# Kernel optimization log

Hardware: AMD Instinct MI355X
Metric: run time of the kernel (lower is better)

The kernel has to match this reference:

```python
import jax, jax.numpy as jnp
import numpy as np

V = 1024      # token vocab
C = 8         # n_codebooks
T = 256       # seg_len
BP = 4        # block_pairs (n_latent_blocks)
K = 512       # latent_vocab_size (codebook entries)
E = 128       # emb_dim
D = 128       # latent_dim / d_model
BETA = 0.05
NB = 6 * BP   # decoder sequence length = 24
NH = 4
HD = D // NH
FF = 512
R = 8
IN_FLAT = NB * D
OUT = T * C * V
B = 32


def setup_inputs() -> dict:
    key = jax.random.key(0)
    ks = jax.random.split(key, 20)
    n = lambda i, shape, s=0.02: jax.random.normal(ks[i], shape, jnp.float32) * s
    return {
        "tokens_prev": jax.random.randint(ks[0], (B, T, C), 0, V, jnp.int32),
        "tokens_curr": jax.random.randint(ks[1], (B, T, C), 0, V, jnp.int32),
        "tokens_next": jax.random.randint(ks[2], (B, T, C), 0, V, jnp.int32),
        "emb": n(3, (V, E)),
        "conv1_w": n(4, (4 * D, E * C, 3)),
        "conv1_b": jnp.zeros((4 * D,), jnp.float32),
        "conv2_w": n(5, (2 * D, 4 * D, 1)),
        "conv2_b": jnp.zeros((2 * D,), jnp.float32),
        "cb_instru": jax.random.uniform(ks[6], (K, D), jnp.float32, -1.0 / K, 1.0 / K),
        "cb_vocal": jax.random.uniform(ks[7], (K, D), jnp.float32, -1.0 / K, 1.0 / K),
        "pos": n(8, (1, NB, D), 1.0),
        "attn_in_w": n(9, (3 * D, D)),
        "attn_in_b": jnp.zeros((3 * D,), jnp.float32),
        "attn_out_w": n(10, (D, D)),
        "attn_out_b": jnp.zeros((D,), jnp.float32),
        "ln1_g": jnp.ones((D,), jnp.float32),
        "ln1_b": jnp.zeros((D,), jnp.float32),
        "lin1_w": n(11, (FF, D)),
        "lin1_b": jnp.zeros((FF,), jnp.float32),
        "lin2_w": n(12, (D, FF)),
        "lin2_b": jnp.zeros((D,), jnp.float32),
        "ln2_g": jnp.ones((D,), jnp.float32),
        "ln2_b": jnp.zeros((D,), jnp.float32),
        "lora_a": n(13, (R, IN_FLAT), 0.01),
        "lora_b": n(14, (OUT, R), 0.01),
    }


def _conv1d(x, w, b, pad):
    # x: (B, Cin, L), w: (Cout, Cin, Kw)
    y = jax.lax.conv_general_dilated(x, w, window_strides=(1,), padding=[(pad, pad)],
                                     dimension_numbers=("NCH", "OIH", "NCH"))
    return y + b[None, :, None]


def _encode(tokens, emb, w1, b1, w2, b2):
    Bb, Tt, Cc = tokens.shape
    x = emb[tokens].reshape(Bb, Tt, -1).transpose(0, 2, 1)       # (B, C*E, T)
    x = jax.nn.relu(_conv1d(x, w1, b1, 1))                        # (B, 4D, T)
    x = jax.nn.relu(_conv1d(x, w2, b2, 0))                        # (B, 2D, T)
    # AdaptiveAvgPool1d(BP) with T % BP == 0 -> mean over contiguous chunks
    x = x.reshape(Bb, 2 * D, BP, Tt // BP).mean(-1).transpose(0, 2, 1)  # (B, BP, 2D)
    return x[..., :D], x[..., D:]


def _vq(z, codebook):
    # z: (B, N, D); eval-mode VQ (no EMA update)
    Bb, N, Dd = z.shape
    flat = z.reshape(-1, Dd)
    dist = (jnp.sum(flat * flat, axis=1, keepdims=True)
            - 2.0 * flat @ codebook.T
            + jnp.sum(codebook * codebook, axis=1))
    codes = jnp.argmin(dist, axis=1)
    z_q = codebook[codes].reshape(Bb, N, Dd)
    commit = jnp.mean((z - jax.lax.stop_gradient(z_q)) ** 2)
    loss = BETA * commit
    z_q_st = z + jax.lax.stop_gradient(z_q - z)
    return z_q_st, codes.reshape(Bb, N), loss


def _layer_norm(x, g, b):
    mu = x.mean(-1, keepdims=True)
    var = ((x - mu) ** 2).mean(-1, keepdims=True)
    return (x - mu) * jax.lax.rsqrt(var + 1e-5) * g + b


def _tf_layer(x, in_w, in_b, out_w, out_b, g1, b1, w1, bb1, w2, bb2, g2, b2):
    # Post-norm TransformerEncoderLayer (relu, eval/no-dropout). x: (B, S, D)
    Bb, S, Dd = x.shape
    qkv = x @ in_w.T + in_b
    q, k, v = jnp.split(qkv, 3, axis=-1)
    q = q.reshape(Bb, S, NH, HD).transpose(0, 2, 1, 3)
    k = k.reshape(Bb, S, NH, HD).transpose(0, 2, 1, 3)
    v = v.reshape(Bb, S, NH, HD).transpose(0, 2, 1, 3)
    attn = jax.nn.softmax(jnp.einsum("bhsd,bhtd->bhst", q, k) / np.sqrt(HD), axis=-1)
    o = jnp.einsum("bhst,bhtd->bhsd", attn, v).transpose(0, 2, 1, 3).reshape(Bb, S, Dd)
    x = _layer_norm(x + o @ out_w.T + out_b, g1, b1)
    ff = jax.nn.relu(x @ w1.T + bb1) @ w2.T + bb2
    return _layer_norm(x + ff, g2, b2)


def reference(tokens_prev, tokens_curr, tokens_next, emb, conv1_w, conv1_b,
              conv2_w, conv2_b, cb_instru, cb_vocal, pos, attn_in_w, attn_in_b,
              attn_out_w, attn_out_b, ln1_g, ln1_b, lin1_w, lin1_b, lin2_w,
              lin2_b, ln2_g, ln2_b, lora_a, lora_b):
    p_i, p_v = _encode(tokens_prev, emb, conv1_w, conv1_b, conv2_w, conv2_b)
    c_i, c_v = _encode(tokens_curr, emb, conv1_w, conv1_b, conv2_w, conv2_b)
    n_i, n_v = _encode(tokens_next, emb, conv1_w, conv1_b, conv2_w, conv2_b)
    p_i_q, _, l1 = _vq(p_i, cb_instru)
    c_i_q, _, l2 = _vq(c_i, cb_instru)
    n_i_q, _, l3 = _vq(n_i, cb_instru)
    p_v_q, _, l4 = _vq(p_v, cb_vocal)
    c_v_q, _, l5 = _vq(c_v, cb_vocal)
    n_v_q, _, l6 = _vq(n_v, cb_vocal)
    vq_loss = l1 + l2 + l3 + l4 + l5 + l6
    z = jnp.concatenate([p_i_q, p_v_q, c_i_q, c_v_q, n_i_q, n_v_q], axis=1)  # (B, 24, D)
    z = z + pos[:, :z.shape[1], :]
    z = _tf_layer(z, attn_in_w, attn_in_b, attn_out_w, attn_out_b,
                  ln1_g, ln1_b, lin1_w, lin1_b, lin2_w, lin2_b, ln2_g, ln2_b)
    Bb = z.shape[0]
    flat = z.reshape(Bb, -1)
    logits = (flat @ lora_a.T) @ lora_b.T          # (B, T*C*V)
    logits = logits.reshape(Bb, T, C, V)
    logp = jax.nn.log_softmax(logits, axis=-1)
    nll = -jnp.take_along_axis(logp, tokens_curr[..., None].astype(jnp.int32), axis=-1)
    recon_loss = nll.mean()
    total_loss = recon_loss + vq_loss
    return total_loss
```

## Files before the change

### kernel.cpp

```cpp
#include <hip/hip_runtime.h>
#include <hip/hip_bf16.h>
#include <cstdint>
#include <cstddef>

typedef __attribute__((ext_vector_type(8))) short short8;
typedef __attribute__((ext_vector_type(4))) float floatx4;


__device__ __forceinline__ ushort f2bf(float f) {
    union { float f; unsigned int u; } x; x.f = f;
    unsigned int r = (x.u + 0x7fffu + ((x.u >> 16) & 1u)) >> 16;
    return (ushort)r;
}
__device__ __forceinline__ float bf2f(ushort u) {
    union { unsigned int u; float f; } x; x.u = ((unsigned int)u) << 16;
    return x.f;
}

__global__ __launch_bounds__(256) void prep_misc(
    const float* __restrict__ emb, const float* __restrict__ w2,
    const float* __restrict__ cbi, const float* __restrict__ cbv,
    ushort* __restrict__ ebf, ushort* __restrict__ w2bf,
    float* __restrict__ cbiT, float* __restrict__ cbvT, float* __restrict__ accum)
{
    int idx = blockIdx.x * 256 + threadIdx.x;
    if (idx < 2) accum[idx] = 0.f;
    if (idx < 131072) {
        ebf[idx] = f2bf(emb[idx]);
    } else if (idx < 262144) {
        int j = idx - 131072;
        w2bf[j] = f2bf(w2[j]);
    } else if (idx < 327680) {
        int j = idx - 262144;
        cbiT[(j & 127) * 512 + (j >> 7)] = cbi[j];
    } else if (idx < 393216) {
        int j = idx - 327680;
        cbvT[(j & 127) * 512 + (j >> 7)] = cbv[j];
    }
}

__global__ __launch_bounds__(256) void prep_w1(
    const float* __restrict__ w1, ushort* __restrict__ w1bf)
{
    int idx = blockIdx.x * 256 + threadIdx.x;
    int e  = idx & 127;
    int co = (idx >> 7) & 511;
    int cc = (idx >> 16) & 7;
    int kw = idx >> 19;
    w1bf[idx] = f2bf(w1[(co * 1024 + cc * 128 + e) * 3 + kw]);
}

__global__ __launch_bounds__(256) void prep_w_tf(
    const float* __restrict__ aiw, const float* __restrict__ aow,
    const float* __restrict__ l1w, const float* __restrict__ l2w,
    ushort* __restrict__ aiwbf, ushort* __restrict__ aowbf,
    ushort* __restrict__ l1wbf, ushort* __restrict__ l2wbf)
{
    int idx = blockIdx.x * 256 + threadIdx.x;
    if (idx < 49152)        aiwbf[idx]          = f2bf(aiw[idx]);
    else if (idx < 65536)   aowbf[idx - 49152]  = f2bf(aow[idx - 49152]);
    else if (idx < 131072)  l1wbf[idx - 65536]  = f2bf(l1w[idx - 65536]);
    else                    l2wbf[idx - 131072] = f2bf(l2w[idx - 131072]);
}

__global__ __launch_bounds__(256) void conv1_mfma(
    const int* __restrict__ tp, const int* __restrict__ tcu, const int* __restrict__ tn,
    const ushort* __restrict__ ebf, const ushort* __restrict__ w1bf,
    const float* __restrict__ b1, ushort* __restrict__ y1)
{
    constexpr int LDA = 136;
    __shared__ ushort As[64 * LDA];
    __shared__ ushort Bs[128 * LDA];
    const int tid = threadIdx.x;
    const int bx = blockIdx.x;
    const int nb = bx & 3, mb = bx >> 2;
    const int set = mb >> 7, bb = (mb >> 2) & 31, t0 = (mb & 3) << 6;
    const int n0 = nb << 7;
    const int* tok = (set == 0) ? tp : ((set == 1) ? tcu : tn);
    const int w = tid >> 6, lane = tid & 63;
    const int rA = lane & 15, q4 = lane >> 4;

    floatx4 acc[4][2];
    for (int mi = 0; mi < 4; ++mi)
        for (int ni = 0; ni < 2; ++ni)
            acc[mi][ni] = (floatx4)(0.0f);

    const int ch = tid & 15;
    for (int kc = 0; kc < 24; ++kc) {
        const int kw = kc >> 3, cc = kc & 7;
        for (int i = 0; i < 4; ++i) {
            const int row = i * 16 + (tid >> 4);
            const int t = t0 + row + kw - 1;
            uint4 val = make_uint4(0u, 0u, 0u, 0u);
            if (t >= 0 && t < 256) {
                const int token = tok[bb * 2048 + t * 8 + cc];
                val = *(const uint4*)(ebf + token * 128 + ch * 8);
            }
            *(uint4*)(As + row * LDA + ch * 8) = val;
        }
        const ushort* wsrc = w1bf + ((size_t)((kw * 8 + cc) * 512 + n0)) * 128;
        for (int i = 0; i < 8; ++i) {
            const int row = i * 16 + (tid >> 4);
            *(uint4*)(Bs + row * LDA + ch * 8) = *(const uint4*)(wsrc + row * 128 + ch * 8);
        }
        __syncthreads();
        for (int ks = 0; ks < 4; ++ks) {
            const int k0 = ks * 32 + q4 * 8;
            short8 a[4], bf[2];
            for (int mi = 0; mi < 4; ++mi)
                a[mi] = *(const short8*)(As + (mi * 16 + rA) * LDA + k0);
            for (int ni = 0; ni < 2; ++ni)
                bf[ni] = *(const short8*)(Bs + ((w * 2 + ni) * 16 + rA) * LDA + k0);
            for (int mi = 0; mi < 4; ++mi)
                for (int ni = 0; ni < 2; ++ni)
                    acc[mi][ni] = __builtin_amdgcn_mfma_f32_16x16x32_bf16(
                        a[mi], bf[ni], acc[mi][ni], 0, 0, 0);
        }
        __syncthreads();
    }
    for (int ni = 0; ni < 2; ++ni) {
        const int co = n0 + (w * 2 + ni) * 16 + rA;
        const float bias = b1[co];
        for (int mi = 0; mi < 4; ++mi) {
            for (int r = 0; r < 4; ++r) {
                const int t = t0 + mi * 16 + q4 * 4 + r;
                float v = acc[mi][ni][r] + bias;
                v = v > 0.f ? v : 0.f;
                y1[((size_t)(set * 32 + bb) * 256 + t) * 512 + co] = f2bf(v);
            }
        }
    }
}

__global__ __launch_bounds__(256) void conv2_mfma(
    const ushort* __restrict__ y1, const ushort* __restrict__ w2bf,
    const float* __restrict__ b2, float* __restrict__ y2)
{
    constexpr int LDA = 136;
    __shared__ ushort As[64 * LDA];
    __shared__ ushort Bs[128 * LDA];
    __shared__ float pool[128];
    const int tid = threadIdx.x;
    const int bx = blockIdx.x;
    const int nb = bx & 1, mb = bx >> 1;
    const int set = mb >> 7, bb = (mb >> 2) & 31, p = mb & 3, t0 = p << 6;
    const int n0 = nb << 7;
    if (tid < 128) pool[tid] = 0.f;
    const int w = tid >> 6, lane = tid & 63;
    const int rA = lane & 15, q4 = lane >> 4;

    floatx4 acc[4][2];
    for (int mi = 0; mi < 4; ++mi)
        for (int ni = 0; ni < 2; ++ni)
            acc[mi][ni] = (floatx4)(0.0f);

    const size_t arowbase = ((size_t)(set * 32 + bb) * 256 + t0) * 512;
    const int ch = tid & 15;
    for (int kc = 0; kc < 4; ++kc) {
        for (int i = 0; i < 4; ++i) {
            const int row = i * 16 + (tid >> 4);
            *(uint4*)(As + row * LDA + ch * 8) =
                *(const uint4*)(y1 + arowbase + (size_t)row * 512 + kc * 128 + ch * 8);
        }
        for (int i = 0; i < 8; ++i) {
            const int row = i * 16 + (tid >> 4);
            *(uint4*)(Bs + row * LDA + ch * 8) =
                *(const uint4*)(w2bf + (size_t)(n0 + row) * 512 + kc * 128 + ch * 8);
        }
        __syncthreads();
        for (int ks = 0; ks < 4; ++ks) {
            const int k0 = ks * 32 + q4 * 8;
            short8 a[4], bf[2];
            for (int mi = 0; mi < 4; ++mi)
                a[mi] = *(const short8*)(As + (mi * 16 + rA) * LDA + k0);
            for (int ni = 0; ni < 2; ++ni)
                bf[ni] = *(const short8*)(Bs + ((w * 2 + ni) * 16 + rA) * LDA + k0);
            for (int mi = 0; mi < 4; ++mi)
                for (int ni = 0; ni < 2; ++ni)
                    acc[mi][ni] = __builtin_amdgcn_mfma_f32_16x16x32_bf16(
                        a[mi], bf[ni], acc[mi][ni], 0, 0, 0);
        }
        __syncthreads();
    }
    for (int ni = 0; ni < 2; ++ni) {
        const int col = (w * 2 + ni) * 16 + rA;
        const float bias = b2[n0 + col];
        float s = 0.f;
        for (int mi = 0; mi < 4; ++mi)
            for (int r = 0; r < 4; ++r) {
                float v = acc[mi][ni][r] + bias;
                s += v > 0.f ? v : 0.f;
            }
        atomicAdd(&pool[col], s);
    }
    __syncthreads();
    if (tid < 128)
        y2[((size_t)(set * 32 + bb) * 4 + p) * 256 + n0 + tid] = pool[tid] * (1.f / 64.f);
}

__global__ __launch_bounds__(256) void vq_kernel(
    const float* __restrict__ y2, const float* __restrict__ cbiT, const float* __restrict__ cbvT,
    const float* __restrict__ cbi, const float* __restrict__ cbv,
    const float* __restrict__ pos, float* __restrict__ ztr, ushort* __restrict__ xbf,
    float* __restrict__ accum)
{
    const int q = blockIdx.x;
    const int tid = threadIdx.x;
    const int set = q >> 7, bb = (q >> 2) & 31, p = q & 3;
    __shared__ float zloc[256];
    __shared__ float bestv[4];
    __shared__ int   besti[4];
    __shared__ int   code_sh[2];
    __shared__ float wsum2[4];
    zloc[tid] = y2[(size_t)q * 256 + tid];
    __syncthreads();
    const int w = tid >> 6, lane = tid & 63;
    const int half = w >> 1, sub = w & 1;
    const float* cbT = half ? cbvT : cbiT;
    const float* zh = zloc + half * 128;
    float best = 1e30f; int bidx = 0x7fffffff;
    for (int rr = 0; rr < 4; ++rr) {
        const int row = sub * 256 + rr * 64 + lane;
        float d2 = 0.f;
        for (int d = 0; d < 128; ++d) {
            float diff = zh[d] - cbT[d * 512 + row];
            d2 += diff * diff;
        }
        if (d2 < best) { best = d2; bidx = row; }
    }
    for (int off = 32; off > 0; off >>= 1) {
        float ov = __shfl_xor(best, off);
        int   oi = __shfl_xor(bidx, off);
        if (ov < best || (ov == best && oi < bidx)) { best = ov; bidx = oi; }
    }
    if (lane == 0) { bestv[w] = best; besti[w] = bidx; }
    __syncthreads();
    if (tid < 2) {
        float v0 = bestv[tid * 2], v1 = bestv[tid * 2 + 1];
        int   i0 = besti[tid * 2], i1 = besti[tid * 2 + 1];
        code_sh[tid] = (v1 < v0 || (v1 == v0 && i1 < i0)) ? i1 : i0;
    }
    __syncthreads();
    const int hh = tid >> 7, d = tid & 127;
    const int code = code_sh[hh];
    const float* cb = hh ? cbv : cbi;
    const float zq = cb[code * 128 + d];
    const float diff = zloc[hh * 128 + d] - zq;
    float sq = diff * diff;
    for (int off = 32; off > 0; off >>= 1) sq += __shfl_xor(sq, off);
    if (lane == 0) wsum2[w] = sq;
    const int s = (set * 2 + hh) * 4 + p;
    const float val = zq + pos[s * 128 + d];
    ztr[((size_t)bb * 24 + s) * 128 + d] = val;
    xbf[((size_t)bb * 24 + s) * 128 + d] = f2bf(val);
    __syncthreads();
    if (tid == 0) atomicAdd(&accum[0], wsum2[0] + wsum2[1] + wsum2[2] + wsum2[3]);
}

template<int KTOT, int NTOT, int RELU, int OUTBF>
__global__ __launch_bounds__(256) void gemm64_kernel(
    const ushort* __restrict__ A, const ushort* __restrict__ Bw,
    const float* __restrict__ bias, void* __restrict__ Co)
{
    constexpr int NBLK = NTOT / 64;
    constexpr int LDA = 136;
    __shared__ ushort As[64 * LDA];
    __shared__ ushort Bs[64 * LDA];
    const int tid = threadIdx.x;
    const int mblk = blockIdx.x / NBLK, nblk = blockIdx.x % NBLK;
    const int m0 = mblk * 64, n0 = nblk * 64;
    const int w = tid >> 6, lane = tid & 63;
    const int rA = lane & 15, q4 = lane >> 4;
    const int ch = tid & 15, rowst = tid >> 4;

    floatx4 acc[4];
    for (int mi = 0; mi < 4; ++mi) acc[mi] = (floatx4)(0.f);

    for (int kc = 0; kc < KTOT / 128; ++kc) {
        for (int i = 0; i < 4; ++i) {
            const int row = i * 16 + rowst;
            *(uint4*)(As + row * LDA + ch * 8) =
                *(const uint4*)(A + (size_t)(m0 + row) * KTOT + kc * 128 + ch * 8);
            *(uint4*)(Bs + row * LDA + ch * 8) =
                *(const uint4*)(Bw + (size_t)(n0 + row) * KTOT + kc * 128 + ch * 8);
        }
        __syncthreads();
        for (int ks = 0; ks < 4; ++ks) {
            const int k0 = ks * 32 + q4 * 8;
            short8 bfr = *(const short8*)(Bs + (w * 16 + rA) * LDA + k0);
            for (int mi = 0; mi < 4; ++mi) {
                short8 a = *(const short8*)(As + (mi * 16 + rA) * LDA + k0);
                acc[mi] = __builtin_amdgcn_mfma_f32_16x16x32_bf16(a, bfr, acc[mi], 0, 0, 0);
            }
        }
        __syncthreads();
    }
    const int col = n0 + w * 16 + rA;
    const float bs = bias[col];
    for (int mi = 0; mi < 4; ++mi) {
        for (int r = 0; r < 4; ++r) {
            const int row = m0 + mi * 16 + q4 * 4 + r;
            float vv = acc[mi][r] + bs;
            if (RELU) vv = vv > 0.f ? vv : 0.f;
            if (OUTBF) ((ushort*)Co)[(size_t)row * NTOT + col] = f2bf(vv);
            else       ((float*)Co)[(size_t)row * NTOT + col]  = vv;
        }
    }
}

template<int KTOT, int WRITE_F32>
__global__ __launch_bounds__(256) void gemm_ln_kernel(
    const ushort* __restrict__ A, const ushort* __restrict__ Bw,
    const float* __restrict__ bias, const float* __restrict__ resid,
    const float* __restrict__ g, const float* __restrict__ beta,
    ushort* __restrict__ outbf, float* __restrict__ outf)
{
    constexpr int LDA = 136;
    __shared__ ushort As[64 * LDA];
    __shared__ ushort Bs[128 * LDA];
    __shared__ float ps[64 * 4], pq[64 * 4], muv[64], invv[64];
    const int tid = threadIdx.x;
    const int m0 = blockIdx.x * 64;
    const int w = tid >> 6, lane = tid & 63;
    const int rA = lane & 15, q4 = lane >> 4;
    const int ch = tid & 15, rowst = tid >> 4;

    floatx4 acc[4][2];
    for (int mi = 0; mi < 4; ++mi)
        for (int ni = 0; ni < 2; ++ni)
            acc[mi][ni] = (floatx4)(0.f);

    for (int kc = 0; kc < KTOT / 128; ++kc) {
        for (int i = 0; i < 4; ++i) {
            const int row = i * 16 + rowst;
            *(uint4*)(As + row * LDA + ch * 8) =
                *(const uint4*)(A + (size_t)(m0 + row) * KTOT + kc * 128 + ch * 8);
        }
        for (int i = 0; i < 8; ++i) {
            const int row = i * 16 + rowst;
            *(uint4*)(Bs + row * LDA + ch * 8) =
                *(const uint4*)(Bw + (size_t)row * KTOT + kc * 128 + ch * 8);
        }
        __syncthreads();
        for (int ks = 0; ks < 4; ++ks) {
            const int k0 = ks * 32 + q4 * 8;
            short8 a[4], bf[2];
            for (int mi = 0; mi < 4; ++mi)
                a[mi] = *(const short8*)(As + (mi * 16 + rA) * LDA + k0);
            for (int ni = 0; ni < 2; ++ni)
                bf[ni] = *(const short8*)(Bs + ((w * 2 + ni) * 16 + rA) * LDA + k0);
            for (int mi = 0; mi < 4; ++mi)
                for (int ni = 0; ni < 2; ++ni)
                    acc[mi][ni] = __builtin_amdgcn_mfma_f32_16x16x32_bf16(
                        a[mi], bf[ni], acc[mi][ni], 0, 0, 0);
        }
        __syncthreads();
    }
    for (int ni = 0; ni < 2; ++ni) {
        const int col = (w * 2 + ni) * 16 + rA;
        const float bs = bias[col];
        for (int mi = 0; mi < 4; ++mi)
            for (int r = 0; r < 4; ++r) {
                const int row = m0 + mi * 16 + q4 * 4 + r;
                acc[mi][ni][r] += bs + resid[(size_t)row * 128 + col];
            }
    }
    for (int mi = 0; mi < 4; ++mi)
        for (int r = 0; r < 4; ++r) {
            float s  = acc[mi][0][r] + acc[mi][1][r];
            float sq = acc[mi][0][r] * acc[mi][0][r] + acc[mi][1][r] * acc[mi][1][r];
            for (int off = 1; off < 16; off <<= 1) {
                s  += __shfl_xor(s, off);
                sq += __shfl_xor(sq, off);
            }
            if (rA == 0) {
                const int rl = mi * 16 + q4 * 4 + r;
                ps[rl * 4 + w] = s;
                pq[rl * 4 + w] = sq;
            }
        }
    __syncthreads();
    if (tid < 64) {
        float s  = ps[tid * 4] + ps[tid * 4 + 1] + ps[tid * 4 + 2] + ps[tid * 4 + 3];
        float sq = pq[tid * 4] + pq[tid * 4 + 1] + pq[tid * 4 + 2] + pq[tid * 4 + 3];
        float mu = s * (1.f / 128.f);
        float var = sq * (1.f / 128.f) - mu * mu;
        muv[tid] = mu;
        invv[tid] = rsqrtf(var + 1e-5f);
    }
    __syncthreads();
    for (int ni = 0; ni < 2; ++ni) {
        const int col = (w * 2 + ni) * 16 + rA;
        const float gg = g[col], bb = beta[col];
        for (int mi = 0; mi < 4; ++mi)
            for (int r = 0; r < 4; ++r) {
                const int rl = mi * 16 + q4 * 4 + r;
                const int row = m0 + rl;
                float v = (acc[mi][ni][r] - muv[rl]) * invv[rl] * gg + bb;
                outbf[(size_t)row * 128 + col] = f2bf(v);
                if (WRITE_F32) outf[(size_t)row * 128 + col] = v;
            }
    }
}

__global__ __launch_bounds__(64) void attn_kernel(
    const float* __restrict__ qkvb, ushort* __restrict__ obuf)
{
    const int bh = blockIdx.x;
    const int b = bh >> 2, h = bh & 3;
    const int tid = threadIdx.x;
    __shared__ float q[24 * 32], k[24 * 32], v[24 * 32], sc[24 * 24];
    for (int i = 0; i < 12; ++i) {
        const int idx = i * 64 + tid;
        const int s = idx >> 5, d = idx & 31;
        const size_t base = ((size_t)(b * 24 + s)) * 384 + h * 32 + d;
        q[idx] = qkvb[base];
        k[idx] = qkvb[base + 128];
        v[idx] = qkvb[base + 256];
    }
    __syncthreads();
    for (int i = 0; i < 9; ++i) {
        const int e = i * 64 + tid;
        const int si = e / 24, j = e - si * 24;
        float a = 0.f;
        for (int d = 0; d < 32; ++d) a += q[si * 32 + d] * k[j * 32 + d];
        sc[si * 24 + j] = a * 0.17677669529663687f;
    }
    __syncthreads();
    if (tid < 24) {
        float* row = sc + tid * 24;
        float m = row[0];
        for (int j = 1; j < 24; ++j) m = row[j] > m ? row[j] : m;
        float ssum = 0.f;
        for (int j = 0; j < 24; ++j) { float e = __expf(row[j] - m); row[j] = e; ssum += e; }
        float inv = 1.f / ssum;
        for (int j = 0; j < 24; ++j) row[j] *= inv;
    }
    __syncthreads();
    for (int i = 0; i < 12; ++i) {
        const int idx = i * 64 + tid;
        const int s = idx >> 5, d = idx & 31;
        float a = 0.f;
        for (int j = 0; j < 24; ++j) a += sc[s * 24 + j] * v[j * 32 + d];
        obuf[((size_t)(b * 24 + s)) * 128 + h * 32 + d] = f2bf(a);
    }
}

__global__ __launch_bounds__(256) void lora_kernel(
    const ushort* __restrict__ zbf, const float* __restrict__ lora_a,
    float* __restrict__ hbuf)
{
    const int b = blockIdx.x;
    const int tid = threadIdx.x;
    const int w = tid >> 6, lane = tid & 63;
    __shared__ float zl[3072];
    for (int idx = tid; idx < 3072; idx += 256) zl[idx] = bf2f(zbf[(size_t)b * 3072 + idx]);
    __syncthreads();
    for (int rr = 0; rr < 2; ++rr) {
        const int r = w + rr * 4;
        float acc = 0.f;
        for (int idx = lane; idx < 3072; idx += 64)
            acc += lora_a[(size_t)r * 3072 + idx] * zl[idx];
        for (int off = 32; off > 0; off >>= 1) acc += __shfl_xor(acc, off);
        if (lane == 0) hbuf[b * 8 + r] = acc;
    }
}

__global__ __launch_bounds__(256) void logits_kernel(
    const float* __restrict__ hbuf, const float* __restrict__ lora_b,
    const int* __restrict__ tokc, float* __restrict__ accum)
{
    const int tid = threadIdx.x;
    const int tcb = blockIdx.x;
    __shared__ float hl[256];
    __shared__ float wsum[4];
    __shared__ float ltok;
    hl[tid] = hbuf[tid];
    float wr[4][8];
    for (int i = 0; i < 4; ++i) {
        const float4* pw = (const float4*)(lora_b + ((size_t)tcb * 1024 + tid + 256 * i) * 8);
        float4 x = pw[0], y = pw[1];
        wr[i][0] = x.x; wr[i][1] = x.y; wr[i][2] = x.z; wr[i][3] = x.w;
        wr[i][4] = y.x; wr[i][5] = y.y; wr[i][6] = y.z; wr[i][7] = y.w;
    }
    __syncthreads();
    float nll = 0.f;
    for (int bb = 0; bb < 32; ++bb) {
        const int tv = tokc[bb * 2048 + tcb];
        const float* h = hl + bb * 8;
        float h0 = h[0], h1 = h[1], h2 = h[2], h3 = h[3];
        float h4 = h[4], h5 = h[5], h6 = h[6], h7 = h[7];
        float sl = 0.f;
        for (int i = 0; i < 4; ++i) {
            float lg = h0 * wr[i][0] + h1 * wr[i][1] + h2 * wr[i][2] + h3 * wr[i][3]
                     + h4 * wr[i][4] + h5 * wr[i][5] + h6 * wr[i][6] + h7 * wr[i][7];
            sl += __expf(lg);
            if (tid + 256 * i == tv) ltok = lg;
        }
        for (int off = 32; off > 0; off >>= 1) sl += __shfl_xor(sl, off);
        if ((tid & 63) == 0) wsum[tid >> 6] = sl;
        __syncthreads();
        if (tid == 0) nll += logf(wsum[0] + wsum[1] + wsum[2] + wsum[3]) - ltok;
        __syncthreads();
    }
    if (tid == 0) atomicAdd(&accum[1], nll);
}

__global__ void finalize_kernel(const float* __restrict__ accum, float* __restrict__ out) {
    out[0] = accum[1] * (1.f / 65536.f) + 0.05f * accum[0] * (1.f / 16384.f);
}

extern "C" void kernel_launch(void* const* d_in, const int* in_sizes, int n_in,
                              void* d_out, int out_size, void* d_ws, size_t ws_size,
                              hipStream_t stream) {
    const int*   tp   = (const int*)d_in[0];
    const int*   tcu  = (const int*)d_in[1];
    const int*   tn   = (const int*)d_in[2];
    const float* emb  = (const float*)d_in[3];
    const float* w1   = (const float*)d_in[4];
    const float* b1   = (const float*)d_in[5];
    const float* w2   = (const float*)d_in[6];
    const float* b2   = (const float*)d_in[7];
    const float* cbi  = (const float*)d_in[8];
    const float* cbv  = (const float*)d_in[9];
    const float* pos  = (const float*)d_in[10];
    const float* aiw  = (const float*)d_in[11];
    const float* aib  = (const float*)d_in[12];
    const float* aow  = (const float*)d_in[13];
    const float* aob  = (const float*)d_in[14];
    const float* g1   = (const float*)d_in[15];
    const float* be1  = (const float*)d_in[16];
    const float* l1w  = (const float*)d_in[17];
    const float* l1b  = (const float*)d_in[18];
    const float* l2w  = (const float*)d_in[19];
    const float* l2b  = (const float*)d_in[20];
    const float* g2   = (const float*)d_in[21];
    const float* be2  = (const float*)d_in[22];
    const float* lra  = (const float*)d_in[23];
    const float* lrb  = (const float*)d_in[24];

    char* wsb = (char*)d_ws;
    ushort* ebf  = (ushort*)(wsb + 0);
    ushort* w1bf = (ushort*)(wsb + 262144);
    ushort* w2bf = (ushort*)(wsb + 3407872);
    float*  cbiT = (float*)(wsb + 3670016);
    float*  cbvT = (float*)(wsb + 3932160);
    ushort* y1   = (ushort*)(wsb + 4194304);
    float*  y2   = (float*)(wsb + 29360128);
    float*  ztr  = (float*)(wsb + 29753344);
    float*  hbuf = (float*)(wsb + 30146560);
    float*  accum= (float*)(wsb + 30147584);
    ushort* aiwbf= (ushort*)(wsb + 30147648);
    ushort* aowbf= (ushort*)(wsb + 30245952);
    ushort* l1wbf= (ushort*)(wsb + 30278720);
    ushort* l2wbf= (ushort*)(wsb + 30409792);
    if (ws_size < 30540864) return;

    float*  qkvb = (float*)(wsb + 4194304);
    ushort* obuf = (ushort*)(wsb + 5373952);
    ushort* x1bf = (ushort*)(wsb + 5570560);
    float*  x1f  = (float*)(wsb + 5767168);
    ushort* hff  = (ushort*)(wsb + 6160384);
    ushort* zbf  = (ushort*)(wsb + 6946816);
    ushort* xbf  = (ushort*)(wsb + 7143424);

    prep_misc<<<1536, 256, 0, stream>>>(emb, w2, cbi, cbv, ebf, w2bf, cbiT, cbvT, accum);
    prep_w1<<<6144, 256, 0, stream>>>(w1, w1bf);
    prep_w_tf<<<768, 256, 0, stream>>>(aiw, aow, l1w, l2w, aiwbf, aowbf, l1wbf, l2wbf);
    conv1_mfma<<<1536, 256, 0, stream>>>(tp, tcu, tn, ebf, w1bf, b1, y1);
    conv2_mfma<<<768, 256, 0, stream>>>(y1, w2bf, b2, y2);
    vq_kernel<<<384, 256, 0, stream>>>(y2, cbiT, cbvT, cbi, cbv, pos, ztr, xbf, accum);
    gemm64_kernel<128, 384, 0, 0><<<72, 256, 0, stream>>>(xbf, aiwbf, aib, qkvb);
    attn_kernel<<<128, 64, 0, stream>>>(qkvb, obuf);
    gemm_ln_kernel<128, 1><<<12, 256, 0, stream>>>(obuf, aowbf, aob, ztr, g1, be1, x1bf, x1f);
    gemm64_kernel<128, 512, 1, 1><<<96, 256, 0, stream>>>(x1bf, l1wbf, l1b, hff);
    gemm_ln_kernel<512, 0><<<12, 256, 0, stream>>>(hff, l2wbf, l2b, x1f, g2, be2, zbf, nullptr);
    lora_kernel<<<32, 256, 0, stream>>>(zbf, lra, hbuf);
    logits_kernel<<<2048, 256, 0, stream>>>(hbuf, lrb, tcu, accum);
    finalize_kernel<<<1, 1, 0, stream>>>(accum, (float*)d_out);
}
```

Measured before the change: 438.6 us.

## Merge prep kernels, enlarge conv tiles with shared embeddings, vectorize VQ, fuse finalize

```diff
diff --git a/kernel.cpp b/kernel.cpp
--- a/kernel.cpp
+++ b/kernel.cpp
@@ -17,113 +17,118 @@
     return x.f;
 }
 
-__global__ __launch_bounds__(256) void prep_misc(
-    const float* __restrict__ emb, const float* __restrict__ w2,
-    const float* __restrict__ cbi, const float* __restrict__ cbv,
-    ushort* __restrict__ ebf, ushort* __restrict__ w2bf,
-    float* __restrict__ cbiT, float* __restrict__ cbvT, float* __restrict__ accum)
+__global__ __launch_bounds__(256) void prep_all(
+    const float* __restrict__ emb, const float* __restrict__ w1,
+    const float* __restrict__ w2, const float* __restrict__ cbi,
+    const float* __restrict__ cbv, const float* __restrict__ aiw,
+    const float* __restrict__ aow, const float* __restrict__ l1w,
+    const float* __restrict__ l2w,
+    ushort* __restrict__ ebf, ushort* __restrict__ w1bf, ushort* __restrict__ w2bf,
+    float* __restrict__ cbiT, float* __restrict__ cbvT,
+    ushort* __restrict__ aiwbf, ushort* __restrict__ aowbf,
+    ushort* __restrict__ l1wbf, ushort* __restrict__ l2wbf,
+    float* __restrict__ accum)
 {
     int idx = blockIdx.x * 256 + threadIdx.x;
-    if (idx < 2) accum[idx] = 0.f;
+    if (idx < 4) accum[idx] = 0.f;
     if (idx < 131072) {
         ebf[idx] = f2bf(emb[idx]);
     } else if (idx < 262144) {
-        int j = idx - 131072;
-        w2bf[j] = f2bf(w2[j]);
+        int j = idx - 131072; w2bf[j] = f2bf(w2[j]);
     } else if (idx < 327680) {
-        int j = idx - 262144;
-        cbiT[(j & 127) * 512 + (j >> 7)] = cbi[j];
+        int j = idx - 262144; cbiT[(j & 127) * 512 + (j >> 7)] = cbi[j];
     } else if (idx < 393216) {
-        int j = idx - 327680;
-        cbvT[(j & 127) * 512 + (j >> 7)] = cbv[j];
-    }
-}
-
-__global__ __launch_bounds__(256) void prep_w1(
-    const float* __restrict__ w1, ushort* __restrict__ w1bf)
-{
-    int idx = blockIdx.x * 256 + threadIdx.x;
-    int e  = idx & 127;
-    int co = (idx >> 7) & 511;
-    int cc = (idx >> 16) & 7;
-    int kw = idx >> 19;
-    w1bf[idx] = f2bf(w1[(co * 1024 + cc * 128 + e) * 3 + kw]);
-}
-
-__global__ __launch_bounds__(256) void prep_w_tf(
-    const float* __restrict__ aiw, const float* __restrict__ aow,
-    const float* __restrict__ l1w, const float* __restrict__ l2w,
-    ushort* __restrict__ aiwbf, ushort* __restrict__ aowbf,
-    ushort* __restrict__ l1wbf, ushort* __restrict__ l2wbf)
-{
-    int idx = blockIdx.x * 256 + threadIdx.x;
-    if (idx < 49152)        aiwbf[idx]          = f2bf(aiw[idx]);
-    else if (idx < 65536)   aowbf[idx - 49152]  = f2bf(aow[idx - 49152]);
-    else if (idx < 131072)  l1wbf[idx - 65536]  = f2bf(l1w[idx - 65536]);
-    else                    l2wbf[idx - 131072] = f2bf(l2w[idx - 131072]);
-}
-
-__global__ __launch_bounds__(256) void conv1_mfma(
+        int j = idx - 327680; cbvT[(j & 127) * 512 + (j >> 7)] = cbv[j];
+    } else if (idx < 442368) {
+        int j = idx - 393216; aiwbf[j] = f2bf(aiw[j]);
+    } else if (idx < 475136) {
+        int j = idx - 442368; aowbf[j] = f2bf(aow[j]);
+    } else if (idx < 540672) {
+        int j = idx - 475136; l1wbf[j] = f2bf(l1w[j]);
+    } else if (idx < 606208) {
+        int j = idx - 540672; l2wbf[j] = f2bf(l2w[j]);
+    } else if (idx < 2179072) {
+        int j = idx - 606208;
+        int e  = j & 127;
+        int co = (j >> 7) & 511;
+        int cc = (j >> 16) & 7;
+        int kw = j >> 19;
+        w1bf[j] = f2bf(w1[(co * 1024 + cc * 128 + e) * 3 + kw]);
+    }
+}
+
+__global__ __launch_bounds__(512, 4) void conv1_mfma(
     const int* __restrict__ tp, const int* __restrict__ tcu, const int* __restrict__ tn,
     const ushort* __restrict__ ebf, const ushort* __restrict__ w1bf,
     const float* __restrict__ b1, ushort* __restrict__ y1)
 {
     constexpr int LDA = 136;
-    __shared__ ushort As[64 * LDA];
+    __shared__ ushort As[130 * LDA];
     __shared__ ushort Bs[128 * LDA];
+    __shared__ int tokL[130 * 8];
     const int tid = threadIdx.x;
     const int bx = blockIdx.x;
     const int nb = bx & 3, mb = bx >> 2;
-    const int set = mb >> 7, bb = (mb >> 2) & 31, t0 = (mb & 3) << 6;
+    const int set = mb >> 6, rem = mb & 63, bb = rem >> 1, t0 = (rem & 1) << 7;
     const int n0 = nb << 7;
     const int* tok = (set == 0) ? tp : ((set == 1) ? tcu : tn);
+
+    for (int idx = tid; idx < 1040; idx += 512) {
+        const int row = idx >> 3, cc = idx & 7;
+        const int gt = t0 + row - 1;
+        tokL[idx] = (gt >= 0 && gt < 256) ? tok[bb * 2048 + gt * 8 + cc] : -1;
+    }
+
     const int w = tid >> 6, lane = tid & 63;
+    const int wm = w & 1, wn = w >> 1;
     const int rA = lane & 15, q4 = lane >> 4;
+    const int ch = tid & 15, rowst = tid >> 4;
 
     floatx4 acc[4][2];
     for (int mi = 0; mi < 4; ++mi)
         for (int ni = 0; ni < 2; ++ni)
             acc[mi][ni] = (floatx4)(0.0f);
 
-    const int ch = tid & 15;
-    for (int kc = 0; kc < 24; ++kc) {
-        const int kw = kc >> 3, cc = kc & 7;
-        for (int i = 0; i < 4; ++i) {
-            const int row = i * 16 + (tid >> 4);
-            const int t = t0 + row + kw - 1;
-            uint4 val = make_uint4(0u, 0u, 0u, 0u);
-            if (t >= 0 && t < 256) {
-                const int token = tok[bb * 2048 + t * 8 + cc];
-                val = *(const uint4*)(ebf + token * 128 + ch * 8);
-            }
-            *(uint4*)(As + row * LDA + ch * 8) = val;
-        }
-        const ushort* wsrc = w1bf + ((size_t)((kw * 8 + cc) * 512 + n0)) * 128;
-        for (int i = 0; i < 8; ++i) {
-            const int row = i * 16 + (tid >> 4);
-            *(uint4*)(Bs + row * LDA + ch * 8) = *(const uint4*)(wsrc + row * 128 + ch * 8);
-        }
-        __syncthreads();
-        for (int ks = 0; ks < 4; ++ks) {
-            const int k0 = ks * 32 + q4 * 8;
-            short8 a[4], bf[2];
-            for (int mi = 0; mi < 4; ++mi)
-                a[mi] = *(const short8*)(As + (mi * 16 + rA) * LDA + k0);
-            for (int ni = 0; ni < 2; ++ni)
-                bf[ni] = *(const short8*)(Bs + ((w * 2 + ni) * 16 + rA) * LDA + k0);
-            for (int mi = 0; mi < 4; ++mi)
+    __syncthreads();
+
+    for (int cc = 0; cc < 8; ++cc) {
+        for (int p = 0; p < 5; ++p) {
+            const int row = p * 32 + rowst;
+            if (row < 130) {
+                const int tk = tokL[row * 8 + cc];
+                uint4 val = make_uint4(0u, 0u, 0u, 0u);
+                if (tk >= 0) val = *(const uint4*)(ebf + tk * 128 + ch * 8);
+                *(uint4*)(As + row * LDA + ch * 8) = val;
+            }
+        }
+        for (int kw = 0; kw < 3; ++kw) {
+            const ushort* wsrc = w1bf + ((size_t)((kw * 8 + cc) * 512 + n0)) * 128;
+            for (int p = 0; p < 4; ++p) {
+                const int row = p * 32 + rowst;
+                *(uint4*)(Bs + row * LDA + ch * 8) = *(const uint4*)(wsrc + row * 128 + ch * 8);
+            }
+            __syncthreads();
+            for (int ks = 0; ks < 4; ++ks) {
+                const int k0 = ks * 32 + q4 * 8;
+                short8 a[4], bfr[2];
+                for (int mi = 0; mi < 4; ++mi)
+                    a[mi] = *(const short8*)(As + (wm * 64 + mi * 16 + rA + kw) * LDA + k0);
                 for (int ni = 0; ni < 2; ++ni)
-                    acc[mi][ni] = __builtin_amdgcn_mfma_f32_16x16x32_bf16(
-                        a[mi], bf[ni], acc[mi][ni], 0, 0, 0);
-        }
-        __syncthreads();
+                    bfr[ni] = *(const short8*)(Bs + (wn * 32 + ni * 16 + rA) * LDA + k0);
+                for (int mi = 0; mi < 4; ++mi)
+                    for (int ni = 0; ni < 2; ++ni)
+                        acc[mi][ni] = __builtin_amdgcn_mfma_f32_16x16x32_bf16(
+                            a[mi], bfr[ni], acc[mi][ni], 0, 0, 0);
+            }
+            __syncthreads();
+        }
     }
     for (int ni = 0; ni < 2; ++ni) {
-        const int co = n0 + (w * 2 + ni) * 16 + rA;
+        const int co = n0 + wn * 32 + ni * 16 + rA;
         const float bias = b1[co];
         for (int mi = 0; mi < 4; ++mi) {
             for (int r = 0; r < 4; ++r) {
-                const int t = t0 + mi * 16 + q4 * 4 + r;
+                const int t = t0 + wm * 64 + mi * 16 + q4 * 4 + r;
                 float v = acc[mi][ni][r] + bias;
                 v = v > 0.f ? v : 0.f;
                 y1[((size_t)(set * 32 + bb) * 256 + t) * 512 + co] = f2bf(v);
@@ -132,22 +137,23 @@
     }
 }
 
-__global__ __launch_bounds__(256) void conv2_mfma(
+__global__ __launch_bounds__(512, 4) void conv2_mfma(
     const ushort* __restrict__ y1, const ushort* __restrict__ w2bf,
     const float* __restrict__ b2, float* __restrict__ y2)
 {
     constexpr int LDA = 136;
-    __shared__ ushort As[64 * LDA];
+    __shared__ ushort As[128 * LDA];
     __shared__ ushort Bs[128 * LDA];
-    __shared__ float pool[128];
+    __shared__ float pool[256];
     const int tid = threadIdx.x;
     const int bx = blockIdx.x;
     const int nb = bx & 1, mb = bx >> 1;
-    const int set = mb >> 7, bb = (mb >> 2) & 31, p = mb & 3, t0 = p << 6;
+    const int set = mb >> 6, rem = mb & 63, bb = rem >> 1, t0 = (rem & 1) << 7;
     const int n0 = nb << 7;
-    if (tid < 128) pool[tid] = 0.f;
     const int w = tid >> 6, lane = tid & 63;
+    const int wm = w & 1, wn = w >> 1;
     const int rA = lane & 15, q4 = lane >> 4;
+    const int ch = tid & 15, rowst = tid >> 4;
 
     floatx4 acc[4][2];
     for (int mi = 0; mi < 4; ++mi)
@@ -155,35 +161,31 @@
             acc[mi][ni] = (floatx4)(0.0f);
 
     const size_t arowbase = ((size_t)(set * 32 + bb) * 256 + t0) * 512;
-    const int ch = tid & 15;
     for (int kc = 0; kc < 4; ++kc) {
-        for (int i = 0; i < 4; ++i) {
-            const int row = i * 16 + (tid >> 4);
+        for (int p = 0; p < 4; ++p) {
+            const int row = p * 32 + rowst;
             *(uint4*)(As + row * LDA + ch * 8) =
                 *(const uint4*)(y1 + arowbase + (size_t)row * 512 + kc * 128 + ch * 8);
-        }
-        for (int i = 0; i < 8; ++i) {
-            const int row = i * 16 + (tid >> 4);
             *(uint4*)(Bs + row * LDA + ch * 8) =
                 *(const uint4*)(w2bf + (size_t)(n0 + row) * 512 + kc * 128 + ch * 8);
         }
         __syncthreads();
         for (int ks = 0; ks < 4; ++ks) {
             const int k0 = ks * 32 + q4 * 8;
-            short8 a[4], bf[2];
+            short8 a[4], bfr[2];
             for (int mi = 0; mi < 4; ++mi)
-                a[mi] = *(const short8*)(As + (mi * 16 + rA) * LDA + k0);
+                a[mi] = *(const short8*)(As + (wm * 64 + mi * 16 + rA) * LDA + k0);
             for (int ni = 0; ni < 2; ++ni)
-                bf[ni] = *(const short8*)(Bs + ((w * 2 + ni) * 16 + rA) * LDA + k0);
+                bfr[ni] = *(const short8*)(Bs + (wn * 32 + ni * 16 + rA) * LDA + k0);
             for (int mi = 0; mi < 4; ++mi)
                 for (int ni = 0; ni < 2; ++ni)
                     acc[mi][ni] = __builtin_amdgcn_mfma_f32_16x16x32_bf16(
-                        a[mi], bf[ni], acc[mi][ni], 0, 0, 0);
+                        a[mi], bfr[ni], acc[mi][ni], 0, 0, 0);
         }
         __syncthreads();
     }
     for (int ni = 0; ni < 2; ++ni) {
-        const int col = (w * 2 + ni) * 16 + rA;
+        const int col = wn * 32 + ni * 16 + rA;
         const float bias = b2[n0 + col];
         float s = 0.f;
         for (int mi = 0; mi < 4; ++mi)
@@ -191,11 +193,16 @@
                 float v = acc[mi][ni][r] + bias;
                 s += v > 0.f ? v : 0.f;
             }
-        atomicAdd(&pool[col], s);
-    }
-    __syncthreads();
-    if (tid < 128)
-        y2[((size_t)(set * 32 + bb) * 4 + p) * 256 + n0 + tid] = pool[tid] * (1.f / 64.f);
+        s += __shfl_xor(s, 16);
+        s += __shfl_xor(s, 32);
+        if (q4 == 0) pool[wm * 128 + col] = s;
+    }
+    __syncthreads();
+    if (tid < 256) {
+        const int wrow = tid >> 7, col = tid & 127;
+        const int p = (t0 >> 6) + wrow;
+        y2[((size_t)(set * 32 + bb) * 4 + p) * 256 + n0 + col] = pool[tid] * (1.f / 64.f);
+    }
 }
 
 __global__ __launch_bounds__(256) void vq_kernel(
@@ -216,18 +223,20 @@
     __syncthreads();
     const int w = tid >> 6, lane = tid & 63;
     const int half = w >> 1, sub = w & 1;
-    const float* cbT = half ? cbvT : cbiT;
+    const float4* cbT4 = (const float4*)(half ? cbvT : cbiT);
     const float* zh = zloc + half * 128;
-    float best = 1e30f; int bidx = 0x7fffffff;
-    for (int rr = 0; rr < 4; ++rr) {
-        const int row = sub * 256 + rr * 64 + lane;
-        float d2 = 0.f;
-        for (int d = 0; d < 128; ++d) {
-            float diff = zh[d] - cbT[d * 512 + row];
-            d2 += diff * diff;
-        }
-        if (d2 < best) { best = d2; bidx = row; }
-    }
+    const int k4 = sub * 64 + lane;
+    float a0 = 0.f, a1 = 0.f, a2 = 0.f, a3 = 0.f;
+    for (int d = 0; d < 128; ++d) {
+        float4 v = cbT4[d * 128 + k4];
+        const float z = zh[d];
+        float d0 = z - v.x, d1 = z - v.y, d2 = z - v.z, d3 = z - v.w;
+        a0 += d0 * d0; a1 += d1 * d1; a2 += d2 * d2; a3 += d3 * d3;
+    }
+    float best = a0; int bidx = k4 * 4;
+    if (a1 < best) { best = a1; bidx = k4 * 4 + 1; }
+    if (a2 < best) { best = a2; bidx = k4 * 4 + 2; }
+    if (a3 < best) { best = a3; bidx = k4 * 4 + 3; }
     for (int off = 32; off > 0; off >>= 1) {
         float ov = __shfl_xor(best, off);
         int   oi = __shfl_xor(bidx, off);
@@ -344,15 +353,15 @@
         __syncthreads();
         for (int ks = 0; ks < 4; ++ks) {
             const int k0 = ks * 32 + q4 * 8;
-            short8 a[4], bf[2];
+            short8 a[4], bfr[2];
             for (int mi = 0; mi < 4; ++mi)
                 a[mi] = *(const short8*)(As + (mi * 16 + rA) * LDA + k0);
             for (int ni = 0; ni < 2; ++ni)
-                bf[ni] = *(const short8*)(Bs + ((w * 2 + ni) * 16 + rA) * LDA + k0);
+                bfr[ni] = *(const short8*)(Bs + ((w * 2 + ni) * 16 + rA) * LDA + k0);
             for (int mi = 0; mi < 4; ++mi)
                 for (int ni = 0; ni < 2; ++ni)
                     acc[mi][ni] = __builtin_amdgcn_mfma_f32_16x16x32_bf16(
-                        a[mi], bf[ni], acc[mi][ni], 0, 0, 0);
+                        a[mi], bfr[ni], acc[mi][ni], 0, 0, 0);
         }
         __syncthreads();
     }
@@ -468,7 +477,7 @@
 
 __global__ __launch_bounds__(256) void logits_kernel(
     const float* __restrict__ hbuf, const float* __restrict__ lora_b,
-    const int* __restrict__ tokc, float* __restrict__ accum)
+    const int* __restrict__ tokc, float* __restrict__ accum, float* __restrict__ out)
 {
     const int tid = threadIdx.x;
     const int tcb = blockIdx.x;
@@ -503,11 +512,16 @@
         if (tid == 0) nll += logf(wsum[0] + wsum[1] + wsum[2] + wsum[3]) - ltok;
         __syncthreads();
     }
-    if (tid == 0) atomicAdd(&accum[1], nll);
-}
-
-__global__ void finalize_kernel(const float* __restrict__ accum, float* __restrict__ out) {
-    out[0] = accum[1] * (1.f / 65536.f) + 0.05f * accum[0] * (1.f / 16384.f);
+    if (tid == 0) {
+        atomicAdd(&accum[1], nll);
+        __threadfence();
+        unsigned int prev = atomicAdd((unsigned int*)(accum + 2), 1u);
+        if (prev == 2047u) {
+            float vq  = atomicAdd(&accum[0], 0.f);
+            float rec = atomicAdd(&accum[1], 0.f);
+            out[0] = rec * (1.f / 65536.f) + 0.05f * vq * (1.f / 16384.f);
+        }
+    }
 }
 
 extern "C" void kernel_launch(void* const* d_in, const int* in_sizes, int n_in,
@@ -564,11 +578,11 @@
     ushort* zbf  = (ushort*)(wsb + 6946816);
     ushort* xbf  = (ushort*)(wsb + 7143424);
 
-    prep_misc<<<1536, 256, 0, stream>>>(emb, w2, cbi, cbv, ebf, w2bf, cbiT, cbvT, accum);
-    prep_w1<<<6144, 256, 0, stream>>>(w1, w1bf);
-    prep_w_tf<<<768, 256, 0, stream>>>(aiw, aow, l1w, l2w, aiwbf, aowbf, l1wbf, l2wbf);
-    conv1_mfma<<<1536, 256, 0, stream>>>(tp, tcu, tn, ebf, w1bf, b1, y1);
-    conv2_mfma<<<768, 256, 0, stream>>>(y1, w2bf, b2, y2);
+    prep_all<<<8512, 256, 0, stream>>>(emb, w1, w2, cbi, cbv, aiw, aow, l1w, l2w,
+                                       ebf, w1bf, w2bf, cbiT, cbvT,
+                                       aiwbf, aowbf, l1wbf, l2wbf, accum);
+    conv1_mfma<<<768, 512, 0, stream>>>(tp, tcu, tn, ebf, w1bf, b1, y1);
+    conv2_mfma<<<384, 512, 0, stream>>>(y1, w2bf, b2, y2);
     vq_kernel<<<384, 256, 0, stream>>>(y2, cbiT, cbvT, cbi, cbv, pos, ztr, xbf, accum);
     gemm64_kernel<128, 384, 0, 0><<<72, 256, 0, stream>>>(xbf, aiwbf, aib, qkvb);
     attn_kernel<<<128, 64, 0, stream>>>(qkvb, obuf);
@@ -576,6 +590,5 @@
     gemm64_kernel<128, 512, 1, 1><<<96, 256, 0, stream>>>(x1bf, l1wbf, l1b, hff);
     gemm_ln_kernel<512, 0><<<12, 256, 0, stream>>>(hff, l2wbf, l2b, x1f, g2, be2, zbf, nullptr);
     lora_kernel<<<32, 256, 0, stream>>>(zbf, lra, hbuf);
-    logits_kernel<<<2048, 256, 0, stream>>>(hbuf, lrb, tcu, accum);
-    finalize_kernel<<<1, 1, 0, stream>>>(accum, (float*)d_out);
-}
+    logits_kernel<<<2048, 256, 0, stream>>>(hbuf, lrb, tcu, accum, (float*)d_out);
+}
```

Result: faster. 404.4 us (-7.8%).
